# Performance work log

Measured on AMD Instinct MI355X. Metric: run time of the kernel, lower is better.

The kernel has to match this reference:

```python
import jax, jax.numpy as jnp
import numpy as np

NUM, K = 5, 3
IN_DIM, D_OUT = 512, 512
N_U, BATCH, GATED_IN = 64, 8192, 576
NB = NUM + K + 1  # 9 basis channels (num+k splines + 1 SiLU base)
TERM_SIZES = (4, 8)
TERM_MULTS = (32768, 16384)  # 4*32768 + 8*16384 = 262144 = D_OUT*IN_DIM
WDIM = 128


def extend_grid(grid, k):
    # grid: (S, num+1) -> (S, num+1+2k), appending k knots each side with uniform spacing h
    h = (grid[:, -1:] - grid[:, :1]) / (grid.shape[1] - 1)
    left = grid[:, :1] + h * jnp.arange(-k, 0, dtype=grid.dtype)
    right = grid[:, -1:] + h * jnp.arange(1, k + 1, dtype=grid.dtype)
    return jnp.concatenate([left, grid, right], axis=1)


def B_batch(x, grid, k):
    # Cox-de-Boor recursion. x: (S, B), grid: (S, G) extended. Returns (S, G-k-1, B).
    xg = x[:, None, :]
    g = grid[:, :, None]
    v = ((xg >= g[:, :-1]) & (xg < g[:, 1:])).astype(x.dtype)
    for p in range(1, k + 1):
        v = (xg - g[:, :-(p + 1)]) / (g[:, p:-1] - g[:, :-(p + 1)]) * v[:, :-1] \
          + (g[:, p + 1:] - xg) / (g[:, p + 1:] - g[:, 1:-p]) * v[:, 1:]
    return v


def lazy_P(terms, mults, perm, w):
    # emlp-style lazy equivariant projector: permute rows, apply small block
    # projectors with multiplicities, un-permute. w: (R, C).
    invperm = jnp.argsort(perm)
    wp = w[perm]
    outs, off = [], 0
    for P, m in zip(terms, mults):
        s = P.shape[0]
        blk = wp[off:off + m * s].reshape(m, s, -1)
        outs.append(jnp.einsum('ij,mjc->mic', P, blk).reshape(m * s, -1))
        off += m * s
    return jnp.concatenate(outs, axis=0)[invperm]


def setup_inputs() -> dict:
    key = jax.random.key(0)
    ks = jax.random.split(key, 12)
    x = jax.random.normal(ks[0], (BATCH, GATED_IN), dtype=jnp.float32)
    grid = jnp.tile(jnp.linspace(-1.0, 1.0, NUM + 1, dtype=jnp.float32)[None, :], (N_U, 1))
    linear_weight = 0.05 * jax.random.normal(ks[1], (D_OUT, NB * IN_DIM), dtype=jnp.float32)
    linear_bias = 0.05 * jax.random.normal(ks[2], (D_OUT,), dtype=jnp.float32)
    P_term_a = 0.3 * jax.random.normal(ks[3], (TERM_SIZES[0], TERM_SIZES[0]), dtype=jnp.float32)
    P_term_b = 0.3 * jax.random.normal(ks[4], (TERM_SIZES[1], TERM_SIZES[1]), dtype=jnp.float32)
    Pb = (1.0 / np.sqrt(D_OUT)) * jax.random.normal(ks[5], (D_OUT, D_OUT), dtype=jnp.float32)
    bi_basis = 0.01 * jax.random.normal(ks[6], (WDIM, D_OUT, D_OUT), dtype=jnp.float32)
    bi_w = jax.random.normal(ks[7], (WDIM,), dtype=jnp.float32)
    u = jnp.sort(jax.random.randint(ks[8], (N_U,), 0, GATED_IN))
    indices = jax.random.randint(ks[9], (IN_DIM,), 0, N_U)
    perm = jax.random.permutation(ks[10], D_OUT * IN_DIM)
    return {"x": x, "grid": grid, "linear_weight": linear_weight, "linear_bias": linear_bias,
            "P_term_a": P_term_a, "P_term_b": P_term_b, "Pb": Pb,
            "bi_basis": bi_basis, "bi_w": bi_w, "u": u, "indices": indices, "perm": perm}


def reference(x, grid, linear_weight, linear_bias, P_term_a, P_term_b, Pb, bi_basis, bi_w, u, indices, perm):
    batch = x.shape[0]
    # gather gate scalars and build spline + base activations
    gs = x[:, u].T                                   # (S, B)
    eg = extend_grid(grid, K)                        # (S, num+1+2k)
    sp = B_batch(gs, eg, K)                          # (S, num+k, B)
    sp = jnp.transpose(sp, (2, 1, 0))                # (B, num+k, S)
    sb = jax.nn.silu(gs).T[:, None, :]               # (B, 1, S)
    g = jnp.concatenate([sp, sb], axis=1)            # (B, NB, S)
    g = g[:, :, indices]                             # (B, NB, in_dim) gather via inverse indices
    acts = (g * x[:, None, :IN_DIM]).reshape(batch, -1)  # (B, NB*in_dim)
    # equivariant weight projection
    w_r = linear_weight.reshape(D_OUT, NB, IN_DIM).transpose(0, 2, 1).reshape(D_OUT * IN_DIM, NB)
    W_r = lazy_P([P_term_a, P_term_b], TERM_MULTS, perm, w_r)
    W = W_r.reshape(D_OUT, IN_DIM, NB).transpose(0, 2, 1).reshape(D_OUT, NB * IN_DIM)
    b = Pb @ linear_bias
    out = acts @ W.T + b                             # (B, D_OUT)
    # bilinear equivariant mix
    bi_W = jnp.einsum('w,wij->ij', bi_w, bi_basis)   # (D_OUT, D_OUT)
    out = 0.1 * (out @ bi_W.T) + out
    return out
```

## Files before the change

### kernel.cpp

```cpp
#include <hip/hip_runtime.h>

#define DI __device__ __forceinline__

typedef __attribute__((ext_vector_type(8))) short short8;
typedef __attribute__((ext_vector_type(4))) float f32x4;

DI ushort f2bf(float f) {
  union { float f; unsigned u; } v; v.f = f;
  unsigned r = v.u + 0x7fffu + ((v.u >> 16) & 1u);
  return (ushort)(r >> 16);
}

DI void gload_lds16(const void* g, void* l) {
  __builtin_amdgcn_global_load_lds((const __attribute__((address_space(1))) void*)g,
                                   (__attribute__((address_space(3))) void*)l, 16, 0, 0);
}

__global__ __launch_bounds__(256) void k_biW(const float2* __restrict__ bb,
                                             const float* __restrict__ bw,
                                             float2* __restrict__ Mf32,
                                             uint* __restrict__ Mbf16) {
  __shared__ float w[128];
  int tid = threadIdx.x;
  if (tid < 128) w[tid] = bw[tid];
  __syncthreads();
  int t = blockIdx.x * 256 + tid;
  const float2* p = bb + t;
  float ax = 0.f, ay = 0.f;
#pragma unroll 8
  for (int k = 0; k < 128; ++k) {
    float2 v = p[(size_t)k * 131072];
    float s = w[k];
    ax += s * v.x; ay += s * v.y;
  }
  int i = t >> 8, j0 = (t & 255) * 2;
  float2 r;
  r.x = 0.1f * ax + (i == j0 + 0 ? 1.f : 0.f);
  r.y = 0.1f * ay + (i == j0 + 1 ? 1.f : 0.f);
  Mf32[t] = r;
  Mbf16[t] = (uint)f2bf(r.x) | ((uint)f2bf(r.y) << 16);
}

__global__ __launch_bounds__(256) void k_matvec(const float* __restrict__ A,
                                                const float* __restrict__ v,
                                                float* __restrict__ y) {
  int o = blockIdx.x * 4 + (threadIdx.x >> 6);
  int lane = threadIdx.x & 63;
  float acc = 0.f;
  for (int k = lane; k < 512; k += 64) acc += A[o * 512 + k] * v[k];
#pragma unroll
  for (int s = 32; s; s >>= 1) acc += __shfl_down(acc, s, 64);
  if (lane == 0) y[o] = acc;
}

__global__ __launch_bounds__(256) void k_lazyP(const float* __restrict__ LW,
                                               const float* __restrict__ Pa,
                                               const float* __restrict__ Pb8,
                                               const int* __restrict__ perm,
                                               ushort* __restrict__ Wt) {
  int q = blockIdx.x * 256 + threadIdx.x;
  int lane = threadIdx.x & 63;
  int r = perm[q];
  int o = r >> 9, ic = r & 511;
  int a_own = o * 4608 + ic;
  if (q < 131072) {
    int ii = lane & 3, g = lane & ~3;
    float pp[4];
#pragma unroll
    for (int j = 0; j < 4; ++j) pp[j] = Pa[ii * 4 + j];
#pragma unroll
    for (int c = 0; c < 9; ++c) {
      float v = LW[a_own + c * 512];
      float acc = 0.f;
#pragma unroll
      for (int j = 0; j < 4; ++j) acc += pp[j] * __shfl(v, g + j, 64);
      Wt[(size_t)(c * 512 + ic) * 512 + o] = f2bf(acc);
    }
  } else {
    int ii = lane & 7, g = lane & ~7;
    float pp[8];
#pragma unroll
    for (int j = 0; j < 8; ++j) pp[j] = Pb8[ii * 8 + j];
#pragma unroll
    for (int c = 0; c < 9; ++c) {
      float v = LW[a_own + c * 512];
      float acc = 0.f;
#pragma unroll
      for (int j = 0; j < 8; ++j) acc += pp[j] * __shfl(v, g + j, 64);
      Wt[(size_t)(c * 512 + ic) * 512 + o] = f2bf(acc);
    }
  }
}

__global__ __launch_bounds__(256) void k_acts(const float* __restrict__ x,
                                              const float* __restrict__ grid,
                                              const int* __restrict__ u,
                                              const int* __restrict__ indices,
                                              ushort* __restrict__ acts) {
  __shared__ float basis[8][64][9];
  __shared__ int sidx[512];
  int tid = threadIdx.x;
  int b0 = blockIdx.x * 8;
  for (int i = tid; i < 512; i += 256) sidx[i] = indices[i];
#pragma unroll
  for (int e0 = 0; e0 < 2; ++e0) {
    int e = e0 * 256 + tid;
    int row = e >> 6, j = e & 63;
    float gs = x[(size_t)(b0 + row) * 576 + u[j]];
    float g0 = grid[j * 6], g5 = grid[j * 6 + 5];
    float h = (g5 - g0) * 0.2f;
    float lo = g0 - 3.f * h;
    float tt = (gs - lo) / h;
#pragma unroll
    for (int n = 0; n < 8; ++n) basis[row][j][n] = 0.f;
    float fc = floorf(tt);
    int c = (int)fc;
    if (c >= 0 && c <= 10) {
      float t = tt - fc;
      float t2 = t * t, t3 = t2 * t;
      float om = 1.f - t;
      float w0 = t3 * (1.f / 6.f);
      float w1 = (1.f + 3.f * t + 3.f * t2 - 3.f * t3) * (1.f / 6.f);
      float w2 = (4.f - 6.f * t2 + 3.f * t3) * (1.f / 6.f);
      float w3 = om * om * om * (1.f / 6.f);
      if (c <= 7) basis[row][j][c] = w0;
      if (c >= 1 && c <= 8) basis[row][j][c - 1] = w1;
      if (c >= 2 && c <= 9) basis[row][j][c - 2] = w2;
      if (c >= 3) basis[row][j][c - 3] = w3;
    }
    basis[row][j][8] = gs / (1.f + __expf(-gs));
  }
  __syncthreads();
#pragma unroll
  for (int rep = 0; rep < 2; ++rep) {
    int e = rep * 256 + tid;
    int row = e >> 6, i0 = (e & 63) * 8;
    size_t xb = (size_t)(b0 + row) * 576;
    float4 xa = *(const float4*)&x[xb + i0];
    float4 xc = *(const float4*)&x[xb + i0 + 4];
    int4 ja = *(const int4*)&sidx[i0];
    int4 jb = *(const int4*)&sidx[i0 + 4];
    size_t ab = (size_t)(b0 + row) * 4608 + i0;
#pragma unroll
    for (int n = 0; n < 9; ++n) {
      short8 hv;
      hv[0] = (short)f2bf(basis[row][ja.x][n] * xa.x);
      hv[1] = (short)f2bf(basis[row][ja.y][n] * xa.y);
      hv[2] = (short)f2bf(basis[row][ja.z][n] * xa.z);
      hv[3] = (short)f2bf(basis[row][ja.w][n] * xa.w);
      hv[4] = (short)f2bf(basis[row][jb.x][n] * xc.x);
      hv[5] = (short)f2bf(basis[row][jb.y][n] * xc.y);
      hv[6] = (short)f2bf(basis[row][jb.z][n] * xc.z);
      hv[7] = (short)f2bf(basis[row][jb.w][n] * xc.w);
      *(short8*)(&acts[ab + (size_t)n * 512]) = hv;
    }
  }
}

template <int BM, int BN>
__global__ __launch_bounds__(256) void gemm_bt(const ushort* __restrict__ A,
                                               const ushort* __restrict__ B,
                                               ushort* __restrict__ Cout,
                                               int N, int Kd) {
  constexpr int BK = 64;
  constexpr int FM = BM / 32;
  constexpr int FN = BN / 32;
  __shared__ __align__(16) ushort Al[2][BM * BK];
  __shared__ __align__(16) ushort Bl[2][BN * BK];
  int tid = threadIdx.x, lane = tid & 63, wid = tid >> 6;
  int wm = wid >> 1, wn = wid & 1;
  int tiles_n = N / BN;
  int per_xcd = gridDim.x >> 3;
  int flat = (blockIdx.x & 7) * per_xcd + (blockIdx.x >> 3);
  int bm = flat / tiles_n, bn = flat % tiles_n;
  long m0 = (long)bm * BM;
  long n0 = (long)bn * BN;
  int swc = ((tid & 7) ^ ((tid >> 3) & 7)) * 8;
  const ushort* agp = A + (m0 + (tid >> 3)) * (long)Kd + swc;
  const ushort* bgp = B + (n0 + (tid >> 3)) * (long)Kd + swc;

#define STAGE(buf, k0)                                                        \
  do {                                                                        \
    _Pragma("unroll")                                                         \
    for (int it = 0; it < BM / 32; ++it)                                      \
      gload_lds16(agp + (it * 32) * (long)Kd + (k0), &Al[buf][(it * 256 + tid) * 8]); \
    _Pragma("unroll")                                                         \
    for (int it = 0; it < BN / 32; ++it)                                      \
      gload_lds16(bgp + (it * 32) * (long)Kd + (k0), &Bl[buf][(it * 256 + tid) * 8]); \
  } while (0)

  f32x4 acc[FM][FN] = {};
  int swz = (lane & 7) << 3;
  int nt = Kd / BK;
  STAGE(0, 0);
  __syncthreads();
  for (int t = 0; t < nt; ++t) {
    int cur = t & 1;
    if (t + 1 < nt) STAGE(cur ^ 1, (t + 1) * BK);
#pragma unroll
    for (int ks = 0; ks < 2; ++ks) {
      int kidx = (ks * 32 + (lane >> 4) * 8) ^ swz;
      short8 a[FM], b[FN];
#pragma unroll
      for (int f = 0; f < FM; ++f)
        a[f] = *(const short8*)&Al[cur][(wm * (FM * 16) + f * 16 + (lane & 15)) * BK + kidx];
#pragma unroll
      for (int f = 0; f < FN; ++f)
        b[f] = *(const short8*)&Bl[cur][(wn * (FN * 16) + f * 16 + (lane & 15)) * BK + kidx];
#pragma unroll
      for (int i = 0; i < FM; ++i)
#pragma unroll
        for (int j = 0; j < FN; ++j)
          acc[i][j] = __builtin_amdgcn_mfma_f32_16x16x32_bf16(a[i], b[j], acc[i][j], 0, 0, 0);
    }
    __syncthreads();
  }
#undef STAGE
#pragma unroll
  for (int i = 0; i < FM; ++i)
#pragma unroll
    for (int j = 0; j < FN; ++j) {
      int row_b = wm * (FM * 16) + i * 16 + ((lane >> 4) * 4);
      long col = n0 + wn * (FN * 16) + j * 16 + (lane & 15);
#pragma unroll
      for (int r = 0; r < 4; ++r)
        Cout[(m0 + row_b + r) * N + col] = f2bf(acc[i][j][r]);
    }
}

__global__ __launch_bounds__(256, 2) void gemm_sk(const ushort* __restrict__ A,
                                                  const ushort* __restrict__ B,
                                                  float* __restrict__ P0,
                                                  float* __restrict__ P1) {
  constexpr int BM = 128, BN = 128, BK = 64, FM = 4, FN = 4;
  const int Kd = 4608, N = 512;
  __shared__ __align__(16) ushort Al[2][BM * BK];
  __shared__ __align__(16) ushort Bl[2][BN * BK];
  int tid = threadIdx.x, lane = tid & 63, wid = tid >> 6;
  int wm = wid >> 1, wn = wid & 1;
  int per_xcd = gridDim.x >> 3;
  int flat = (blockIdx.x & 7) * per_xcd + (blockIdx.x >> 3);
  int kb = flat >> 8;
  int rem = flat & 255;
  int bm = rem >> 2, bn = rem & 3;
  long m0 = (long)bm * BM;
  long n0 = (long)bn * BN;
  int kbase = kb * (Kd / 2);
  float* Pout = kb ? P1 : P0;

  int swc = ((tid & 7) ^ ((tid >> 3) & 7)) * 8;
  const ushort* agp = A + (m0 + (tid >> 3)) * (long)Kd + kbase + swc;
  const ushort* bgp = B + (n0 + (tid >> 3)) * (long)Kd + kbase + swc;

#define STAGE(buf, k0)                                                        \
  do {                                                                        \
    _Pragma("unroll")                                                         \
    for (int it = 0; it < 4; ++it)                                            \
      gload_lds16(agp + (it * 32) * (long)Kd + (k0), &Al[buf][(it * 256 + tid) * 8]); \
    _Pragma("unroll")                                                         \
    for (int it = 0; it < 4; ++it)                                            \
      gload_lds16(bgp + (it * 32) * (long)Kd + (k0), &Bl[buf][(it * 256 + tid) * 8]); \
  } while (0)

  f32x4 acc[FM][FN] = {};
  int swz = (lane & 7) << 3;
  const int nt = (Kd / 2) / BK;
  STAGE(0, 0);
  __syncthreads();
  for (int t = 0; t < nt; ++t) {
    int cur = t & 1;
    if (t + 1 < nt) STAGE(cur ^ 1, (t + 1) * BK);
#pragma unroll
    for (int ks = 0; ks < 2; ++ks) {
      int kidx = (ks * 32 + (lane >> 4) * 8) ^ swz;
      short8 a[FM], b[FN];
#pragma unroll
      for (int f = 0; f < FM; ++f)
        a[f] = *(const short8*)&Al[cur][(wm * 64 + f * 16 + (lane & 15)) * BK + kidx];
#pragma unroll
      for (int f = 0; f < FN; ++f)
        b[f] = *(const short8*)&Bl[cur][(wn * 64 + f * 16 + (lane & 15)) * BK + kidx];
#pragma unroll
      for (int i = 0; i < FM; ++i)
#pragma unroll
        for (int j = 0; j < FN; ++j)
          acc[i][j] = __builtin_amdgcn_mfma_f32_16x16x32_bf16(a[i], b[j], acc[i][j], 0, 0, 0);
    }
    __syncthreads();
  }
#undef STAGE
#pragma unroll
  for (int i = 0; i < FM; ++i)
#pragma unroll
    for (int j = 0; j < FN; ++j) {
      int row_b = wm * 64 + i * 16 + ((lane >> 4) * 4);
      long col = n0 + wn * 64 + j * 16 + (lane & 15);
#pragma unroll
      for (int r = 0; r < 4; ++r)
        Pout[(m0 + row_b + r) * N + col] = acc[i][j][r];
    }
}

__global__ __launch_bounds__(256) void k_reduce(float4* __restrict__ P0,
                                                const float4* __restrict__ P1,
                                                const float4* __restrict__ b2) {
  int t = blockIdx.x * 256 + threadIdx.x;
#pragma unroll
  for (int rep = 0; rep < 2; ++rep) {
    int e = rep * 524288 + t;
    float4 a = P0[e], b = P1[e], c = b2[e & 127];
    a.x += b.x + c.x; a.y += b.y + c.y; a.z += b.z + c.z; a.w += b.w + c.w;
    P0[e] = a;
  }
}

extern "C" void kernel_launch(void* const* d_in, const int* in_sizes, int n_in,
                              void* d_out, int out_size, void* d_ws, size_t ws_size,
                              hipStream_t stream) {
  const float* x        = (const float*)d_in[0];
  const float* grid     = (const float*)d_in[1];
  const float* LW       = (const float*)d_in[2];
  const float* lb       = (const float*)d_in[3];
  const float* Pa       = (const float*)d_in[4];
  const float* Pb8      = (const float*)d_in[5];
  const float* Pbm      = (const float*)d_in[6];
  const float* bi_basis = (const float*)d_in[7];
  const float* bi_w     = (const float*)d_in[8];
  const int*   u        = (const int*)d_in[9];
  const int*   indices  = (const int*)d_in[10];
  const int*   perm     = (const int*)d_in[11];
  float* out = (float*)d_out;
  char* ws = (char*)d_ws;

  float*  Mf32  = (float*)(ws + 0);
  ushort* Mbf16 = (ushort*)(ws + 1048576);
  float*  tvec  = (float*)(ws + 1572864);
  float*  b2    = (float*)(ws + 1576960);
  ushort* Wt    = (ushort*)(ws + 2097152);
  ushort* W2    = (ushort*)(ws + 6815744);
  ushort* acts  = (ushort*)(ws + 11534336);
  float*  P1    = (float*)(ws + 87031808);

  k_biW<<<512, 256, 0, stream>>>((const float2*)bi_basis, bi_w, (float2*)Mf32, (uint*)Mbf16);
  k_matvec<<<128, 256, 0, stream>>>(Pbm, lb, tvec);
  k_matvec<<<128, 256, 0, stream>>>(Mf32, tvec, b2);
  k_lazyP<<<1024, 256, 0, stream>>>(LW, Pa, Pb8, perm, Wt);
  gemm_bt<128, 128><<<(512 / 128) * (4608 / 128), 256, 0, stream>>>(
      Mbf16, Wt, W2, 4608, 512);
  k_acts<<<1024, 256, 0, stream>>>(x, grid, u, indices, acts);
  gemm_sk<<<512, 256, 0, stream>>>(acts, W2, out, P1);
  k_reduce<<<2048, 256, 0, stream>>>((float4*)out, (const float4*)P1, (const float4*)b2);
}
```

Baseline: 167.2 us.

## Merge prep kernels into one launch and split main GEMM K four ways

Folds the bilinear-weight, activation-building, lazy projector and bias matvec kernels into one block-range-dispatched prep kernel, removing several launches and letting independent work overlap. The main GEMM moves from a 2-way to a 4-way split-K with BK=32, a new LDS swizzle and a higher occupancy bound, which doubles the block count. The reduce kernel now sums four partial buffers. The cost is extra partial-buffer traffic and a larger LDS footprint in the merged kernel, since every block reserves the shared memory of all branches.

```diff
diff --git a/kernel.cpp b/kernel.cpp
--- a/kernel.cpp
+++ b/kernel.cpp
@@ -16,29 +16,144 @@
                                    (__attribute__((address_space(3))) void*)l, 16, 0, 0);
 }
 
-__global__ __launch_bounds__(256) void k_biW(const float2* __restrict__ bb,
-                                             const float* __restrict__ bw,
-                                             float2* __restrict__ Mf32,
-                                             uint* __restrict__ Mbf16) {
-  __shared__ float w[128];
+__global__ __launch_bounds__(256) void k_prep(const float* __restrict__ x,
+                                              const float* __restrict__ grid,
+                                              const float* __restrict__ LW,
+                                              const float* __restrict__ lb,
+                                              const float* __restrict__ Pa,
+                                              const float* __restrict__ Pb8,
+                                              const float* __restrict__ Pbm,
+                                              const float2* __restrict__ bb,
+                                              const float* __restrict__ bw,
+                                              const int* __restrict__ u,
+                                              const int* __restrict__ indices,
+                                              const int* __restrict__ perm,
+                                              float2* __restrict__ Mf32,
+                                              uint* __restrict__ Mbf16,
+                                              ushort* __restrict__ Wt,
+                                              ushort* __restrict__ acts,
+                                              float* __restrict__ tvec) {
+  int bid = blockIdx.x;
   int tid = threadIdx.x;
-  if (tid < 128) w[tid] = bw[tid];
-  __syncthreads();
-  int t = blockIdx.x * 256 + tid;
-  const float2* p = bb + t;
-  float ax = 0.f, ay = 0.f;
+  if (bid < 512) {
+    __shared__ float w[128];
+    if (tid < 128) w[tid] = bw[tid];
+    __syncthreads();
+    int t = bid * 256 + tid;
+    const float2* p = bb + t;
+    float ax = 0.f, ay = 0.f;
 #pragma unroll 8
-  for (int k = 0; k < 128; ++k) {
-    float2 v = p[(size_t)k * 131072];
-    float s = w[k];
-    ax += s * v.x; ay += s * v.y;
+    for (int k = 0; k < 128; ++k) {
+      float2 v = p[(size_t)k * 131072];
+      float s = w[k];
+      ax += s * v.x; ay += s * v.y;
+    }
+    int i = t >> 8, j0 = (t & 255) * 2;
+    float2 r;
+    r.x = 0.1f * ax + (i == j0 + 0 ? 1.f : 0.f);
+    r.y = 0.1f * ay + (i == j0 + 1 ? 1.f : 0.f);
+    Mf32[t] = r;
+    Mbf16[t] = (uint)f2bf(r.x) | ((uint)f2bf(r.y) << 16);
+  } else if (bid < 1536) {
+    __shared__ float basis[8][64][9];
+    __shared__ int sidx[512];
+    int b0 = (bid - 512) * 8;
+    for (int i = tid; i < 512; i += 256) sidx[i] = indices[i];
+#pragma unroll
+    for (int e0 = 0; e0 < 2; ++e0) {
+      int e = e0 * 256 + tid;
+      int row = e >> 6, j = e & 63;
+      float gs = x[(size_t)(b0 + row) * 576 + u[j]];
+      float g0 = grid[j * 6], g5 = grid[j * 6 + 5];
+      float h = (g5 - g0) * 0.2f;
+      float lo = g0 - 3.f * h;
+      float tt = (gs - lo) / h;
+#pragma unroll
+      for (int n = 0; n < 8; ++n) basis[row][j][n] = 0.f;
+      float fc = floorf(tt);
+      int c = (int)fc;
+      if (c >= 0 && c <= 10) {
+        float t = tt - fc;
+        float t2 = t * t, t3 = t2 * t;
+        float om = 1.f - t;
+        float w0 = t3 * (1.f / 6.f);
+        float w1 = (1.f + 3.f * t + 3.f * t2 - 3.f * t3) * (1.f / 6.f);
+        float w2 = (4.f - 6.f * t2 + 3.f * t3) * (1.f / 6.f);
+        float w3 = om * om * om * (1.f / 6.f);
+        if (c <= 7) basis[row][j][c] = w0;
+        if (c >= 1 && c <= 8) basis[row][j][c - 1] = w1;
+        if (c >= 2 && c <= 9) basis[row][j][c - 2] = w2;
+        if (c >= 3) basis[row][j][c - 3] = w3;
+      }
+      basis[row][j][8] = gs / (1.f + __expf(-gs));
+    }
+    __syncthreads();
+#pragma unroll
+    for (int rep = 0; rep < 2; ++rep) {
+      int e = rep * 256 + tid;
+      int row = e >> 6, i0 = (e & 63) * 8;
+      size_t xb = (size_t)(b0 + row) * 576;
+      float4 xa = *(const float4*)&x[xb + i0];
+      float4 xc = *(const float4*)&x[xb + i0 + 4];
+      int4 ja = *(const int4*)&sidx[i0];
+      int4 jb = *(const int4*)&sidx[i0 + 4];
+      size_t ab = (size_t)(b0 + row) * 4608 + i0;
+#pragma unroll
+      for (int n = 0; n < 9; ++n) {
+        short8 hv;
+        hv[0] = (short)f2bf(basis[row][ja.x][n] * xa.x);
+        hv[1] = (short)f2bf(basis[row][ja.y][n] * xa.y);
+        hv[2] = (short)f2bf(basis[row][ja.z][n] * xa.z);
+        hv[3] = (short)f2bf(basis[row][ja.w][n] * xa.w);
+        hv[4] = (short)f2bf(basis[row][jb.x][n] * xc.x);
+        hv[5] = (short)f2bf(basis[row][jb.y][n] * xc.y);
+        hv[6] = (short)f2bf(basis[row][jb.z][n] * xc.z);
+        hv[7] = (short)f2bf(basis[row][jb.w][n] * xc.w);
+        *(short8*)(&acts[ab + (size_t)n * 512]) = hv;
+      }
+    }
+  } else if (bid < 2560) {
+    int q = (bid - 1536) * 256 + tid;
+    int lane = tid & 63;
+    int r = perm[q];
+    int o = r >> 9, ic = r & 511;
+    int a_own = o * 4608 + ic;
+    if (q < 131072) {
+      int ii = lane & 3, g = lane & ~3;
+      float pp[4];
+#pragma unroll
+      for (int j = 0; j < 4; ++j) pp[j] = Pa[ii * 4 + j];
+#pragma unroll
+      for (int c = 0; c < 9; ++c) {
+        float v = LW[a_own + c * 512];
+        float acc = 0.f;
+#pragma unroll
+        for (int j = 0; j < 4; ++j) acc += pp[j] * __shfl(v, g + j, 64);
+        Wt[(size_t)(c * 512 + ic) * 512 + o] = f2bf(acc);
+      }
+    } else {
+      int ii = lane & 7, g = lane & ~7;
+      float pp[8];
+#pragma unroll
+      for (int j = 0; j < 8; ++j) pp[j] = Pb8[ii * 8 + j];
+#pragma unroll
+      for (int c = 0; c < 9; ++c) {
+        float v = LW[a_own + c * 512];
+        float acc = 0.f;
+#pragma unroll
+        for (int j = 0; j < 8; ++j) acc += pp[j] * __shfl(v, g + j, 64);
+        Wt[(size_t)(c * 512 + ic) * 512 + o] = f2bf(acc);
+      }
+    }
+  } else {
+    int o = (bid - 2560) * 4 + (tid >> 6);
+    int lane = tid & 63;
+    float acc = 0.f;
+    for (int k = lane; k < 512; k += 64) acc += Pbm[o * 512 + k] * lb[k];
+#pragma unroll
+    for (int s = 32; s; s >>= 1) acc += __shfl_down(acc, s, 64);
+    if (lane == 0) tvec[o] = acc;
   }
-  int i = t >> 8, j0 = (t & 255) * 2;
-  float2 r;
-  r.x = 0.1f * ax + (i == j0 + 0 ? 1.f : 0.f);
-  r.y = 0.1f * ay + (i == j0 + 1 ? 1.f : 0.f);
-  Mf32[t] = r;
-  Mbf16[t] = (uint)f2bf(r.x) | ((uint)f2bf(r.y) << 16);
 }
 
 __global__ __launch_bounds__(256) void k_matvec(const float* __restrict__ A,
@@ -51,110 +166,6 @@
 #pragma unroll
   for (int s = 32; s; s >>= 1) acc += __shfl_down(acc, s, 64);
   if (lane == 0) y[o] = acc;
-}
-
-__global__ __launch_bounds__(256) void k_lazyP(const float* __restrict__ LW,
-                                               const float* __restrict__ Pa,
-                                               const float* __restrict__ Pb8,
-                                               const int* __restrict__ perm,
-                                               ushort* __restrict__ Wt) {
-  int q = blockIdx.x * 256 + threadIdx.x;
-  int lane = threadIdx.x & 63;
-  int r = perm[q];
-  int o = r >> 9, ic = r & 511;
-  int a_own = o * 4608 + ic;
-  if (q < 131072) {
-    int ii = lane & 3, g = lane & ~3;
-    float pp[4];
-#pragma unroll
-    for (int j = 0; j < 4; ++j) pp[j] = Pa[ii * 4 + j];
-#pragma unroll
-    for (int c = 0; c < 9; ++c) {
-      float v = LW[a_own + c * 512];
-      float acc = 0.f;
-#pragma unroll
-      for (int j = 0; j < 4; ++j) acc += pp[j] * __shfl(v, g + j, 64);
-      Wt[(size_t)(c * 512 + ic) * 512 + o] = f2bf(acc);
-    }
-  } else {
-    int ii = lane & 7, g = lane & ~7;
-    float pp[8];
-#pragma unroll
-    for (int j = 0; j < 8; ++j) pp[j] = Pb8[ii * 8 + j];
-#pragma unroll
-    for (int c = 0; c < 9; ++c) {
-      float v = LW[a_own + c * 512];
-      float acc = 0.f;
-#pragma unroll
-      for (int j = 0; j < 8; ++j) acc += pp[j] * __shfl(v, g + j, 64);
-      Wt[(size_t)(c * 512 + ic) * 512 + o] = f2bf(acc);
-    }
-  }
-}
-
-__global__ __launch_bounds__(256) void k_acts(const float* __restrict__ x,
-                                              const float* __restrict__ grid,
-                                              const int* __restrict__ u,
-                                              const int* __restrict__ indices,
-                                              ushort* __restrict__ acts) {
-  __shared__ float basis[8][64][9];
-  __shared__ int sidx[512];
-  int tid = threadIdx.x;
-  int b0 = blockIdx.x * 8;
-  for (int i = tid; i < 512; i += 256) sidx[i] = indices[i];
-#pragma unroll
-  for (int e0 = 0; e0 < 2; ++e0) {
-    int e = e0 * 256 + tid;
-    int row = e >> 6, j = e & 63;
-    float gs = x[(size_t)(b0 + row) * 576 + u[j]];
-    float g0 = grid[j * 6], g5 = grid[j * 6 + 5];
-    float h = (g5 - g0) * 0.2f;
-    float lo = g0 - 3.f * h;
-    float tt = (gs - lo) / h;
-#pragma unroll
-    for (int n = 0; n < 8; ++n) basis[row][j][n] = 0.f;
-    float fc = floorf(tt);
-    int c = (int)fc;
-    if (c >= 0 && c <= 10) {
-      float t = tt - fc;
-      float t2 = t * t, t3 = t2 * t;
-      float om = 1.f - t;
-      float w0 = t3 * (1.f / 6.f);
-      float w1 = (1.f + 3.f * t + 3.f * t2 - 3.f * t3) * (1.f / 6.f);
-      float w2 = (4.f - 6.f * t2 + 3.f * t3) * (1.f / 6.f);
-      float w3 = om * om * om * (1.f / 6.f);
-      if (c <= 7) basis[row][j][c] = w0;
-      if (c >= 1 && c <= 8) basis[row][j][c - 1] = w1;
-      if (c >= 2 && c <= 9) basis[row][j][c - 2] = w2;
-      if (c >= 3) basis[row][j][c - 3] = w3;
-    }
-    basis[row][j][8] = gs / (1.f + __expf(-gs));
-  }
-  __syncthreads();
-#pragma unroll
-  for (int rep = 0; rep < 2; ++rep) {
-    int e = rep * 256 + tid;
-    int row = e >> 6, i0 = (e & 63) * 8;
-    size_t xb = (size_t)(b0 + row) * 576;
-    float4 xa = *(const float4*)&x[xb + i0];
-    float4 xc = *(const float4*)&x[xb + i0 + 4];
-    int4 ja = *(const int4*)&sidx[i0];
-    int4 jb = *(const int4*)&sidx[i0 + 4];
-    size_t ab = (size_t)(b0 + row) * 4608 + i0;
-#pragma unroll
-    for (int n = 0; n < 9; ++n) {
-      short8 hv;
-      hv[0] = (short)f2bf(basis[row][ja.x][n] * xa.x);
-      hv[1] = (short)f2bf(basis[row][ja.y][n] * xa.y);
-      hv[2] = (short)f2bf(basis[row][ja.z][n] * xa.z);
-      hv[3] = (short)f2bf(basis[row][ja.w][n] * xa.w);
-      hv[4] = (short)f2bf(basis[row][jb.x][n] * xc.x);
-      hv[5] = (short)f2bf(basis[row][jb.y][n] * xc.y);
-      hv[6] = (short)f2bf(basis[row][jb.z][n] * xc.z);
-      hv[7] = (short)f2bf(basis[row][jb.w][n] * xc.w);
-      *(short8*)(&acts[ab + (size_t)n * 512]) = hv;
-    }
-  }
 }
 
 template <int BM, int BN>
@@ -179,7 +190,7 @@
   const ushort* agp = A + (m0 + (tid >> 3)) * (long)Kd + swc;
   const ushort* bgp = B + (n0 + (tid >> 3)) * (long)Kd + swc;
 
-#define STAGE(buf, k0)                                                        \
+#define STAGE64(buf, k0)                                                      \
   do {                                                                        \
     _Pragma("unroll")                                                         \
     for (int it = 0; it < BM / 32; ++it)                                      \
@@ -192,11 +203,11 @@
   f32x4 acc[FM][FN] = {};
   int swz = (lane & 7) << 3;
   int nt = Kd / BK;
-  STAGE(0, 0);
+  STAGE64(0, 0);
   __syncthreads();
   for (int t = 0; t < nt; ++t) {
     int cur = t & 1;
-    if (t + 1 < nt) STAGE(cur ^ 1, (t + 1) * BK);
+    if (t + 1 < nt) STAGE64(cur ^ 1, (t + 1) * BK);
 #pragma unroll
     for (int ks = 0; ks < 2; ++ks) {
       int kidx = (ks * 32 + (lane >> 4) * 8) ^ swz;
@@ -215,7 +226,7 @@
     }
     __syncthreads();
   }
-#undef STAGE
+#undef STAGE64
 #pragma unroll
   for (int i = 0; i < FM; ++i)
 #pragma unroll
@@ -228,67 +239,66 @@
     }
 }
 
-__global__ __launch_bounds__(256, 2) void gemm_sk(const ushort* __restrict__ A,
+__global__ __launch_bounds__(256, 4) void gemm_sk(const ushort* __restrict__ A,
                                                   const ushort* __restrict__ B,
                                                   float* __restrict__ P0,
-                                                  float* __restrict__ P1) {
-  constexpr int BM = 128, BN = 128, BK = 64, FM = 4, FN = 4;
+                                                  float* __restrict__ P1,
+                                                  float* __restrict__ P2,
+                                                  float* __restrict__ P3) {
+  constexpr int BM = 128, BN = 128, BK = 32, FM = 4, FN = 4;
   const int Kd = 4608, N = 512;
   __shared__ __align__(16) ushort Al[2][BM * BK];
   __shared__ __align__(16) ushort Bl[2][BN * BK];
   int tid = threadIdx.x, lane = tid & 63, wid = tid >> 6;
   int wm = wid >> 1, wn = wid & 1;
-  int per_xcd = gridDim.x >> 3;
-  int flat = (blockIdx.x & 7) * per_xcd + (blockIdx.x >> 3);
-  int kb = flat >> 8;
-  int rem = flat & 255;
-  int bm = rem >> 2, bn = rem & 3;
-  long m0 = (long)bm * BM;
-  long n0 = (long)bn * BN;
-  int kbase = kb * (Kd / 2);
-  float* Pout = kb ? P1 : P0;
-
-  int swc = ((tid & 7) ^ ((tid >> 3) & 7)) * 8;
-  const ushort* agp = A + (m0 + (tid >> 3)) * (long)Kd + kbase + swc;
-  const ushort* bgp = B + (n0 + (tid >> 3)) * (long)Kd + kbase + swc;
-
-#define STAGE(buf, k0)                                                        \
+  int flat = (blockIdx.x & 7) * 128 + (blockIdx.x >> 3);
+  int bm = flat >> 4, kb = (flat >> 2) & 3, bn = flat & 3;
+  long m0 = (long)bm * BM, n0 = (long)bn * BN;
+  int kbase = kb * 1152;
+  float* Pout = kb == 0 ? P0 : kb == 1 ? P1 : kb == 2 ? P2 : P3;
+
+  int r0 = tid >> 2, c0 = tid & 3;
+  int swc = (c0 ^ ((r0 >> 1) & 3)) * 8;
+  const ushort* agp = A + (m0 + r0) * (long)Kd + kbase + swc;
+  const ushort* bgp = B + (n0 + r0) * (long)Kd + kbase + swc;
+
+#define STAGE32(buf, k0)                                                      \
   do {                                                                        \
     _Pragma("unroll")                                                         \
-    for (int it = 0; it < 4; ++it)                                            \
-      gload_lds16(agp + (it * 32) * (long)Kd + (k0), &Al[buf][(it * 256 + tid) * 8]); \
+    for (int it = 0; it < 2; ++it)                                            \
+      gload_lds16(agp + (it * 64) * (long)Kd + (k0), &Al[buf][it * 2048 + tid * 8]); \
     _Pragma("unroll")                                                         \
-    for (int it = 0; it < 4; ++it)                                            \
-      gload_lds16(bgp + (it * 32) * (long)Kd + (k0), &Bl[buf][(it * 256 + tid) * 8]); \
+    for (int it = 0; it < 2; ++it)                                            \
+      gload_lds16(bgp + (it * 64) * (long)Kd + (k0), &Bl[buf][it * 2048 + tid * 8]); \
   } while (0)
 
   f32x4 acc[FM][FN] = {};
-  int swz = (lane & 7) << 3;
-  const int nt = (Kd / 2) / BK;
-  STAGE(0, 0);
+  const int nt = 1152 / BK;
+  int e0 = lane >> 4;
+  STAGE32(0, 0);
   __syncthreads();
   for (int t = 0; t < nt; ++t) {
     int cur = t & 1;
-    if (t + 1 < nt) STAGE(cur ^ 1, (t + 1) * BK);
-#pragma unroll
-    for (int ks = 0; ks < 2; ++ks) {
-      int kidx = (ks * 32 + (lane >> 4) * 8) ^ swz;
-      short8 a[FM], b[FN];
-#pragma unroll
-      for (int f = 0; f < FM; ++f)
-        a[f] = *(const short8*)&Al[cur][(wm * 64 + f * 16 + (lane & 15)) * BK + kidx];
-#pragma unroll
-      for (int f = 0; f < FN; ++f)
-        b[f] = *(const short8*)&Bl[cur][(wn * 64 + f * 16 + (lane & 15)) * BK + kidx];
-#pragma unroll
-      for (int i = 0; i < FM; ++i)
-#pragma unroll
-        for (int j = 0; j < FN; ++j)
-          acc[i][j] = __builtin_amdgcn_mfma_f32_16x16x32_bf16(a[i], b[j], acc[i][j], 0, 0, 0);
-    }
+    if (t + 1 < nt) STAGE32(cur ^ 1, (t + 1) * BK);
+    short8 a[FM], b[FN];
+#pragma unroll
+    for (int f = 0; f < FM; ++f) {
+      int fr = wm * 64 + f * 16 + (lane & 15);
+      a[f] = *(const short8*)&Al[cur][fr * BK + ((e0 ^ ((fr >> 1) & 3)) * 8)];
+    }
+#pragma unroll
+    for (int f = 0; f < FN; ++f) {
+      int fr = wn * 64 + f * 16 + (lane & 15);
+      b[f] = *(const short8*)&Bl[cur][fr * BK + ((e0 ^ ((fr >> 1) & 3)) * 8)];
+    }
+#pragma unroll
+    for (int i = 0; i < FM; ++i)
+#pragma unroll
+      for (int j = 0; j < FN; ++j)
+        acc[i][j] = __builtin_amdgcn_mfma_f32_16x16x32_bf16(a[i], b[j], acc[i][j], 0, 0, 0);
     __syncthreads();
   }
-#undef STAGE
+#undef STAGE32
 #pragma unroll
   for (int i = 0; i < FM; ++i)
 #pragma unroll
@@ -303,13 +313,18 @@
 
 __global__ __launch_bounds__(256) void k_reduce(float4* __restrict__ P0,
                                                 const float4* __restrict__ P1,
+                                                const float4* __restrict__ P2,
+                                                const float4* __restrict__ P3,
                                                 const float4* __restrict__ b2) {
   int t = blockIdx.x * 256 + threadIdx.x;
 #pragma unroll
   for (int rep = 0; rep < 2; ++rep) {
     int e = rep * 524288 + t;
-    float4 a = P0[e], b = P1[e], c = b2[e & 127];
-    a.x += b.x + c.x; a.y += b.y + c.y; a.z += b.z + c.z; a.w += b.w + c.w;
+    float4 a = P0[e], b = P1[e], c = P2[e], d = P3[e], bb = b2[e & 127];
+    a.x += b.x + c.x + d.x + bb.x;
+    a.y += b.y + c.y + d.y + bb.y;
+    a.z += b.z + c.z + d.z + bb.z;
+    a.w += b.w + c.w + d.w + bb.w;
     P0[e] = a;
   }
 }
@@ -340,14 +355,17 @@
   ushort* W2    = (ushort*)(ws + 6815744);
   ushort* acts  = (ushort*)(ws + 11534336);
   float*  P1    = (float*)(ws + 87031808);
-
-  k_biW<<<512, 256, 0, stream>>>((const float2*)bi_basis, bi_w, (float2*)Mf32, (uint*)Mbf16);
-  k_matvec<<<128, 256, 0, stream>>>(Pbm, lb, tvec);
+  float*  P2    = (float*)(ws + 103809024);
+  float*  P3    = (float*)(ws + 120586240);
+
+  k_prep<<<2688, 256, 0, stream>>>(x, grid, LW, lb, Pa, Pb8, Pbm,
+                                   (const float2*)bi_basis, bi_w, u, indices, perm,
+                                   (float2*)Mf32, (uint*)Mbf16, Wt, acts, tvec);
   k_matvec<<<128, 256, 0, stream>>>(Mf32, tvec, b2);
-  k_lazyP<<<1024, 256, 0, stream>>>(LW, Pa, Pb8, perm, Wt);
   gemm_bt<128, 128><<<(512 / 128) * (4608 / 128), 256, 0, stream>>>(
       Mbf16, Wt, W2, 4608, 512);
-  k_acts<<<1024, 256, 0, stream>>>(x, grid, u, indices, acts);
-  gemm_sk<<<512, 256, 0, stream>>>(acts, W2, out, P1);
-  k_reduce<<<2048, 256, 0, stream>>>((float4*)out, (const float4*)P1, (const float4*)b2);
-}
+  gemm_sk<<<1024, 256, 0, stream>>>(acts, W2, out, P1, P2, P3);
+  k_reduce<<<2048, 256, 0, stream>>>((float4*)out, (const float4*)P1,
+                                     (const float4*)P2, (const float4*)P3,
+                                     (const float4*)b2);
+}
```

After: 183.6 us. 1.1x slower.

## Fuse bias into split-K GEMM, remap block order, shrink weight GEMM tile

Applied to the files above, without the earlier changes.

The bias add moves from the reduce kernel into the split-K GEMM epilogue of the first K half, so the reduce only sums the two partials. The split-K block mapping changes so that both K halves and all four N tiles of an M block land on the same XCD, which may improve L2 reuse of the A rows. The weight-projection GEMM tile drops from 128x128 to 64x128, doubling its block count for better CU occupancy. The k_biW unroll factor also rises from 8 to 16.

```diff
diff --git a/kernel.cpp b/kernel.cpp
--- a/kernel.cpp
+++ b/kernel.cpp
@@ -15,6 +15,7 @@
   __builtin_amdgcn_global_load_lds((const __attribute__((address_space(1))) void*)g,
                                    (__attribute__((address_space(3))) void*)l, 16, 0, 0);
 }
+
 
 __global__ __launch_bounds__(256) void k_biW(const float2* __restrict__ bb,
                                              const float* __restrict__ bw,
@@ -27,7 +28,7 @@
   int t = blockIdx.x * 256 + tid;
   const float2* p = bb + t;
   float ax = 0.f, ay = 0.f;
-#pragma unroll 8
+#pragma unroll 16
   for (int k = 0; k < 128; ++k) {
     float2 v = p[(size_t)k * 131072];
     float s = w[k];
@@ -179,7 +180,7 @@
   const ushort* agp = A + (m0 + (tid >> 3)) * (long)Kd + swc;
   const ushort* bgp = B + (n0 + (tid >> 3)) * (long)Kd + swc;
 
-#define STAGE(buf, k0)                                                        \
+#define STAGE64(buf, k0)                                                      \
   do {                                                                        \
     _Pragma("unroll")                                                         \
     for (int it = 0; it < BM / 32; ++it)                                      \
@@ -192,11 +193,11 @@
   f32x4 acc[FM][FN] = {};
   int swz = (lane & 7) << 3;
   int nt = Kd / BK;
-  STAGE(0, 0);
+  STAGE64(0, 0);
   __syncthreads();
   for (int t = 0; t < nt; ++t) {
     int cur = t & 1;
-    if (t + 1 < nt) STAGE(cur ^ 1, (t + 1) * BK);
+    if (t + 1 < nt) STAGE64(cur ^ 1, (t + 1) * BK);
 #pragma unroll
     for (int ks = 0; ks < 2; ++ks) {
       int kidx = (ks * 32 + (lane >> 4) * 8) ^ swz;
@@ -215,7 +216,7 @@
     }
     __syncthreads();
   }
-#undef STAGE
+#undef STAGE64
 #pragma unroll
   for (int i = 0; i < FM; ++i)
 #pragma unroll
@@ -230,6 +231,7 @@
 
 __global__ __launch_bounds__(256, 2) void gemm_sk(const ushort* __restrict__ A,
                                                   const ushort* __restrict__ B,
+                                                  const float* __restrict__ b2,
                                                   float* __restrict__ P0,
                                                   float* __restrict__ P1) {
   constexpr int BM = 128, BN = 128, BK = 64, FM = 4, FN = 4;
@@ -238,14 +240,10 @@
   __shared__ __align__(16) ushort Bl[2][BN * BK];
   int tid = threadIdx.x, lane = tid & 63, wid = tid >> 6;
   int wm = wid >> 1, wn = wid & 1;
-  int per_xcd = gridDim.x >> 3;
-  int flat = (blockIdx.x & 7) * per_xcd + (blockIdx.x >> 3);
-  int kb = flat >> 8;
-  int rem = flat & 255;
-  int bm = rem >> 2, bn = rem & 3;
-  long m0 = (long)bm * BM;
-  long n0 = (long)bn * BN;
-  int kbase = kb * (Kd / 2);
+  int flat = (blockIdx.x & 7) * 64 + (blockIdx.x >> 3);
+  int bm = flat >> 3, kb = (flat >> 2) & 1, bn = flat & 3;
+  long m0 = (long)bm * BM, n0 = (long)bn * BN;
+  int kbase = kb * 2304;
   float* Pout = kb ? P1 : P0;
 
   int swc = ((tid & 7) ^ ((tid >> 3) & 7)) * 8;
@@ -264,7 +262,7 @@
 
   f32x4 acc[FM][FN] = {};
   int swz = (lane & 7) << 3;
-  const int nt = (Kd / 2) / BK;
+  const int nt = 2304 / BK;
   STAGE(0, 0);
   __syncthreads();
   for (int t = 0; t < nt; ++t) {
@@ -295,21 +293,21 @@
     for (int j = 0; j < FN; ++j) {
       int row_b = wm * 64 + i * 16 + ((lane >> 4) * 4);
       long col = n0 + wn * 64 + j * 16 + (lane & 15);
+      float bv = (kb == 0) ? b2[col] : 0.f;
 #pragma unroll
       for (int r = 0; r < 4; ++r)
-        Pout[(m0 + row_b + r) * N + col] = acc[i][j][r];
+        Pout[(m0 + row_b + r) * N + col] = acc[i][j][r] + bv;
     }
 }
 
 __global__ __launch_bounds__(256) void k_reduce(float4* __restrict__ P0,
-                                                const float4* __restrict__ P1,
-                                                const float4* __restrict__ b2) {
+                                                const float4* __restrict__ P1) {
   int t = blockIdx.x * 256 + threadIdx.x;
 #pragma unroll
   for (int rep = 0; rep < 2; ++rep) {
     int e = rep * 524288 + t;
-    float4 a = P0[e], b = P1[e], c = b2[e & 127];
-    a.x += b.x + c.x; a.y += b.y + c.y; a.z += b.z + c.z; a.w += b.w + c.w;
+    float4 a = P0[e], b = P1[e];
+    a.x += b.x; a.y += b.y; a.z += b.z; a.w += b.w;
     P0[e] = a;
   }
 }
@@ -345,9 +343,9 @@
   k_matvec<<<128, 256, 0, stream>>>(Pbm, lb, tvec);
   k_matvec<<<128, 256, 0, stream>>>(Mf32, tvec, b2);
   k_lazyP<<<1024, 256, 0, stream>>>(LW, Pa, Pb8, perm, Wt);
-  gemm_bt<128, 128><<<(512 / 128) * (4608 / 128), 256, 0, stream>>>(
+  gemm_bt<64, 128><<<(512 / 64) * (4608 / 128), 256, 0, stream>>>(
       Mbf16, Wt, W2, 4608, 512);
   k_acts<<<1024, 256, 0, stream>>>(x, grid, u, indices, acts);
-  gemm_sk<<<512, 256, 0, stream>>>(acts, W2, out, P1);
-  k_reduce<<<2048, 256, 0, stream>>>((float4*)out, (const float4*)P1, (const float4*)b2);
-}
+  gemm_sk<<<512, 256, 0, stream>>>(acts, W2, b2, out, P1);
+  k_reduce<<<2048, 256, 0, stream>>>((float4*)out, (const float4*)P1);
+}
```

New measurement: 167.6 us. Within noise of the previous version (+0.2%).
